# Performance work log

Measured on AMD Instinct MI355X. Metric: run time of the kernel, lower is better.

Reference implementation:

```python
import jax, jax.numpy as jnp
import numpy as np

B, T, NX, NXS, H, NY, NYS = 16384, 60, 4, 3, 64, 4, 3


def _lstm(x, h0, c0, Wih, Whh, bih, bhh):
    """PyTorch-convention LSTM (gate order i,f,g,o). x: [B,T,X]. Returns (hs [B,T,H], hT, cT)."""
    # precompute input contribution for all timesteps: [T,B,4H]
    xg = jnp.transpose(jnp.einsum('btx,gx->btg', x, Wih) + (bih + bhh), (1, 0, 2))

    def step(carry, xg_t):
        h, c = carry
        g = xg_t + h @ Whh.T
        i, f, gg, o = jnp.split(g, 4, axis=-1)
        c = jax.nn.sigmoid(f) * c + jax.nn.sigmoid(i) * jnp.tanh(gg)
        h = jax.nn.sigmoid(o) * jnp.tanh(c)
        return (h, c), h

    (hT, cT), hs = jax.lax.scan(step, (h0, c0), xg)
    return jnp.transpose(hs, (1, 0, 2)), hT, cT


def setup_inputs() -> dict:
    key = jax.random.key(0)
    ks = jax.random.split(key, 24)
    w = lambda k, shp: (jax.random.normal(k, shp, jnp.float32) * 0.1)
    return {
        'inputs_main': jax.random.normal(ks[0], (B, T, NX), jnp.float32),
        'inputs_aux': jax.random.normal(ks[1], (B, NXS), jnp.float32),
        'hx2': jax.random.normal(ks[2], (B, H), jnp.float32),
        'cx2': jax.random.normal(ks[3], (B, H), jnp.float32),
        'Ws1': w(ks[4], (H, NXS)), 'bs1': w(ks[5], (H,)),
        'Ws2': w(ks[6], (H, NXS)), 'bs2': w(ks[7], (H,)),
        'Wih1': w(ks[8], (4 * H, NX)), 'Whh1': w(ks[9], (4 * H, H)),
        'bih1': w(ks[10], (4 * H,)), 'bhh1': w(ks[11], (4 * H,)),
        'Wih2': w(ks[12], (4 * H, H)), 'Whh2': w(ks[13], (4 * H, H)),
        'bih2': w(ks[14], (4 * H,)), 'bhh2': w(ks[15], (4 * H,)),
        'Wlat': w(ks[16], (H, H)), 'blat': w(ks[17], (H,)),
        'Wout': w(ks[18], (NY, H)), 'bout': w(ks[19], (NY,)),
        'Wsfc': w(ks[20], (NYS, H)), 'bsfc': w(ks[21], (NYS,)),
    }


def reference(inputs_main, inputs_aux, hx2, cx2, Ws1, bs1, Ws2, bs2,
              Wih1, Whh1, bih1, bhh1, Wih2, Whh2, bih2, bhh2,
              Wlat, blat, Wout, bout, Wsfc, bsfc):
    # surface MLPs -> initial LSTM1 state (h raw, c tanh'd)
    hx = inputs_aux @ Ws1.T + bs1
    cx = jnp.tanh(inputs_aux @ Ws2.T + bs2)
    # run LSTM1 top-down (flipped levels)
    x1 = jnp.flip(inputs_main, axis=1)
    rnn1out, _, _ = _lstm(x1, hx, cx, Wih1, Whh1, bih1, bhh1)
    # flip back and run LSTM2 bottom-up with (hx2, cx2)
    # (the original calls rnn2 twice; only the second call's result is used)
    rnn1out_f = jnp.flip(rnn1out, axis=1)
    rnn2out, last_h, _ = _lstm(rnn1out_f, hx2, cx2, Wih2, Whh2, bih2, bhh2)
    # intermediate MLP + output head
    lat = rnn2out @ Wlat.T + blat                # [B,T,H]
    out = lat @ Wout.T + bout                    # [B,T,NY]
    out_sfc = jax.nn.relu(last_h @ Wsfc.T + bsfc)  # [B,NYS]
    return out, out_sfc
```

## Files before the change

### kernel.cpp

```cpp
#include <hip/hip_runtime.h>
#include <hip/hip_bf16.h>

#define BB 16384
#define TT 60

typedef short bf16x8 __attribute__((ext_vector_type(8)));
typedef float f32x4 __attribute__((ext_vector_type(4)));

__device__ __forceinline__ unsigned short f2bs(float f) {
    __hip_bfloat16 h = __float2bfloat16(f);
    return __builtin_bit_cast(unsigned short, h);
}

__device__ __forceinline__ unsigned cvtpk2(float lo, float hi) {
    unsigned r;
    asm("v_cvt_pk_bf16_f32 %0, %1, %2" : "=v"(r) : "v"(lo), "v"(hi));
    return r;
}

__device__ __forceinline__ void lstm_cell(float xi, float xf, float xg, float xo,
                                          float& c, float& h) {
    xi = __builtin_amdgcn_fmed3f(xi, -17.f, 17.f);
    xf = __builtin_amdgcn_fmed3f(xf, -17.f, 17.f);
    xo = __builtin_amdgcn_fmed3f(xo, -17.f, 17.f);
    xg = __builtin_amdgcn_fmed3f(xg, -11.f, 11.f);
    const float ei = __expf(-xi), ef = __expf(-xf), eo = __expf(-xo), eg = __expf(2.f * xg);
    const float di = 1.f + ei, df = 1.f + ef, dd = 1.f + eo, dg = 1.f + eg;
    const float a = di * df, b = dd * dg;
    const float R = __builtin_amdgcn_rcpf(a * b);
    const float si = df * b * R;
    const float sf = di * b * R;
    const float so = a * dg * R;
    const float tg = (eg - 1.f) * (a * dd) * R;
    const float cn = sf * c + si * tg;
    c = cn;
    const float tc = __builtin_amdgcn_fmed3f(cn, -11.f, 11.f);
    const float ec = __expf(2.f * tc);
    const float th = (ec - 1.f) * __builtin_amdgcn_rcpf(ec + 1.f);
    h = so * th;
}

#define STEP_BARRIER() do {                                   \
    asm volatile("s_waitcnt lgkmcnt(0)" ::: "memory");        \
    __builtin_amdgcn_s_barrier();                             \
    __builtin_amdgcn_sched_barrier(0);                        \
} while (0)

__device__ __forceinline__ bf16x8 pack8(float4 a, float4 b) {
    bf16x8 r;
    r[0] = (short)f2bs(a.x); r[1] = (short)f2bs(a.y);
    r[2] = (short)f2bs(a.z); r[3] = (short)f2bs(a.w);
    r[4] = (short)f2bs(b.x); r[5] = (short)f2bs(b.y);
    r[6] = (short)f2bs(b.z); r[7] = (short)f2bs(b.w);
    return r;
}

__global__ __launch_bounds__(256, 2) void k_lstm1(
    const float* __restrict__ xmain, const float* __restrict__ aux,
    const float* __restrict__ Ws1, const float* __restrict__ bs1,
    const float* __restrict__ Ws2, const float* __restrict__ bs2,
    const float* __restrict__ Wih1, const float* __restrict__ Whh1,
    const float* __restrict__ bih1, const float* __restrict__ bhh1,
    unsigned short* __restrict__ rnn1t)
{
    __shared__ unsigned short hB[2 * 4096];

    const int tid = threadIdx.x;
    {
        unsigned int* p32 = (unsigned int*)hB;
        #pragma unroll
        for (int e = 0; e < 16; ++e) p32[tid + 256 * e] = 0;
    }
    const int hj = tid >> 6, lane = tid & 63;
    const int row16 = lane & 15, quad = lane >> 4;
    const int b0 = blockIdx.x * 32;
    const int swz = (row16 & 7) << 3;

    bf16x8 wf[4][3];
    float fb[4];
    #pragma unroll
    for (int i = 0; i < 4; ++i) {
        const int g = (hj + 4 * i) * 16 + row16;
        const float* wr = Whh1 + g * 64 + quad * 8;
        wf[i][0] = pack8(*(const float4*)wr, *(const float4*)(wr + 4));
        wf[i][1] = pack8(*(const float4*)(wr + 32), *(const float4*)(wr + 36));
        float4 z4 = {0.f, 0.f, 0.f, 0.f};
        float4 xw = z4;
        if (quad == 0) xw = *(const float4*)(Wih1 + g * 4);
        wf[i][2] = pack8(xw, z4);
        fb[i] = bih1[g] + bhh1[g];
    }
    __syncthreads();

    const int j = hj * 16 + row16;
    const unsigned oA0 = (unsigned)(((row16 * 128 + 0 + quad * 8) ^ swz) * 2);
    const unsigned oA1 = (unsigned)(((row16 * 128 + 32 + quad * 8) ^ swz) * 2);
    const unsigned oA2 = (unsigned)(((row16 * 128 + 64 + quad * 8) ^ swz) * 2);
    unsigned oW[4];
    #pragma unroll
    for (int r = 0; r < 4; ++r) {
        const int m = quad * 4 + r;
        oW[r] = (unsigned)(((m * 128 + j) ^ ((m & 7) << 3)) * 2);
    }
    const unsigned oX = (unsigned)(((lane * 128 + 64) ^ ((lane & 7) << 3)) * 2);
    char* const hBb = (char*)hB;

    const float w10 = Ws1[j * 3], w11 = Ws1[j * 3 + 1], w12 = Ws1[j * 3 + 2], sb1v = bs1[j];
    const float w20 = Ws2[j * 3], w21 = Ws2[j * 3 + 1], w22 = Ws2[j * 3 + 2], sb2v = bs2[j];
    f32x4 cc[2];
    #pragma unroll
    for (int mh = 0; mh < 2; ++mh) {
        #pragma unroll
        for (int r = 0; r < 4; ++r) {
            const int m = mh * 16 + quad * 4 + r;
            const float a0v = aux[(b0 + m) * 3], a1v = aux[(b0 + m) * 3 + 1], a2v = aux[(b0 + m) * 3 + 2];
            float h0 = w10 * a0v + w11 * a1v + w12 * a2v + sb1v;
            float c0in = w20 * a0v + w21 * a1v + w22 * a2v + sb2v;
            c0in = __builtin_amdgcn_fmed3f(c0in, -11.f, 11.f);
            const float e0 = __expf(2.f * c0in);
            cc[mh][r] = (e0 - 1.f) * __builtin_amdgcn_rcpf(e0 + 1.f);
            *(unsigned short*)(hBb + oW[r] + mh * 4096) = f2bs(h0);
        }
    }
    if (hj == 2 && lane < 32) {
        float4 xv = ((const float4*)xmain)[(size_t)(b0 + lane) * TT + 59];
        uint2 p2 = { cvtpk2(xv.x, xv.y), cvtpk2(xv.z, xv.w) };
        *(uint2*)(hBb + oX) = p2;
    }
    __syncthreads();

    const float4* px = (const float4*)xmain + (size_t)(b0 + lane) * TT + 58;
    unsigned short* pst = rnn1t + ((size_t)60 * BB + b0 + ((hj >> 1) << 4) + row16) * 64 + ((hj & 1) << 5) + quad * 8;

    unsigned pofs = 0;
    #pragma unroll 1
    for (int s = 0; s < TT; ++s) {
        char* hbP = hBb + pofs;
        char* hbN = hBb + (pofs ^ 8192);
        float4 xv;
        if (hj == 2 && lane < 32 && s < TT - 1) xv = *px;
        bf16x8 a0[2], a1[2], a2[2];
        #pragma unroll
        for (int mh = 0; mh < 2; ++mh) {
            a0[mh] = *(const bf16x8*)(hbP + oA0 + mh * 4096);
            a1[mh] = *(const bf16x8*)(hbP + oA1 + mh * 4096);
            a2[mh] = *(const bf16x8*)(hbP + oA2 + mh * 4096);
        }
        if (s > 0) {
            bf16x8 sv = (hj == 0) ? a0[0] : (hj == 1) ? a1[0] : (hj == 2) ? a0[1] : a1[1];
            *(bf16x8*)pst = sv;
        }
        pst -= (size_t)BB * 64;
        px -= 1;

        f32x4 ac[2][4];
        #pragma unroll
        for (int mh = 0; mh < 2; ++mh)
            #pragma unroll
            for (int i = 0; i < 4; ++i) { f32x4 v = {fb[i], fb[i], fb[i], fb[i]}; ac[mh][i] = v; }
        #pragma unroll
        for (int mh = 0; mh < 2; ++mh) {
            #pragma unroll
            for (int i = 0; i < 4; ++i) {
                ac[mh][i] = __builtin_amdgcn_mfma_f32_16x16x32_bf16(a0[mh], wf[i][0], ac[mh][i], 0, 0, 0);
                ac[mh][i] = __builtin_amdgcn_mfma_f32_16x16x32_bf16(a1[mh], wf[i][1], ac[mh][i], 0, 0, 0);
                ac[mh][i] = __builtin_amdgcn_mfma_f32_16x16x32_bf16(a2[mh], wf[i][2], ac[mh][i], 0, 0, 0);
            }
        }
        #pragma unroll
        for (int mh = 0; mh < 2; ++mh) {
            float hr[4];
            #pragma unroll
            for (int r = 0; r < 4; ++r) {
                float cr = cc[mh][r];
                lstm_cell(ac[mh][0][r], ac[mh][1][r], ac[mh][2][r], ac[mh][3][r], cr, hr[r]);
                cc[mh][r] = cr;
            }
            const unsigned u01 = cvtpk2(hr[0], hr[1]);
            const unsigned u23 = cvtpk2(hr[2], hr[3]);
            *(unsigned short*)(hbN + oW[0] + mh * 4096) = (unsigned short)u01;
            *(unsigned short*)(hbN + oW[1] + mh * 4096) = (unsigned short)(u01 >> 16);
            *(unsigned short*)(hbN + oW[2] + mh * 4096) = (unsigned short)u23;
            *(unsigned short*)(hbN + oW[3] + mh * 4096) = (unsigned short)(u23 >> 16);
        }
        if (hj == 2 && lane < 32 && s < TT - 1) {
            uint2 p2 = { cvtpk2(xv.x, xv.y), cvtpk2(xv.z, xv.w) };
            *(uint2*)(hbN + oX) = p2;
        }
        STEP_BARRIER();
        pofs ^= 8192;
    }
    {
        char* hbP = hBb + pofs;
        bf16x8 sv;
        if (hj == 0)      sv = *(const bf16x8*)(hbP + oA0);
        else if (hj == 1) sv = *(const bf16x8*)(hbP + oA1);
        else if (hj == 2) sv = *(const bf16x8*)(hbP + oA0 + 4096);
        else              sv = *(const bf16x8*)(hbP + oA1 + 4096);
        *(bf16x8*)&rnn1t[((size_t)(b0 + ((hj >> 1) << 4) + row16)) * 64 + ((hj & 1) << 5) + quad * 8] = sv;
    }
}

__global__ __launch_bounds__(256, 2) void k_lstm2(
    const unsigned short* __restrict__ rnn1t,
    const float* __restrict__ hx2, const float* __restrict__ cx2,
    const float* __restrict__ Wih2, const float* __restrict__ Whh2,
    const float* __restrict__ bih2, const float* __restrict__ bhh2,
    const float* __restrict__ Wlat, const float* __restrict__ blat,
    const float* __restrict__ Wout, const float* __restrict__ bout,
    const float* __restrict__ Wsfc, const float* __restrict__ bsfc,
    float* __restrict__ out)
{
    __shared__ unsigned short hB[2 * 4096];
    __shared__ unsigned short whead[16 * 64];

    const int tid = threadIdx.x;
    {
        unsigned int* w32 = (unsigned int*)whead;
        w32[tid] = 0; w32[tid + 256] = 0;
    }
    const int hj = tid >> 6, lane = tid & 63;
    const int row16 = lane & 15, quad = lane >> 4;
    const int b0 = blockIdx.x * 32;
    const int swz = (row16 & 7) << 3;

    bf16x8 wf[4][4];
    float fb[4];
    #pragma unroll
    for (int i = 0; i < 4; ++i) {
        const int g = (hj + 4 * i) * 16 + row16;
        const float* wh = Whh2 + g * 64 + quad * 8;
        const float* wi = Wih2 + g * 64 + quad * 8;
        wf[i][0] = pack8(*(const float4*)wh, *(const float4*)(wh + 4));
        wf[i][1] = pack8(*(const float4*)(wh + 32), *(const float4*)(wh + 36));
        wf[i][2] = pack8(*(const float4*)wi, *(const float4*)(wi + 4));
        wf[i][3] = pack8(*(const float4*)(wi + 32), *(const float4*)(wi + 36));
        fb[i] = bih2[g] + bhh2[g];
    }
    float bcomb = 0.f;
    if (row16 < 4) {
        float s = 0.f;
        for (int jj = 0; jj < 64; ++jj) s += Wout[row16 * 64 + jj] * blat[jj];
        bcomb = s + bout[row16];
    } else if (row16 < 7) {
        bcomb = bsfc[row16 - 4];
    }
    __syncthreads();

    {
        const int o = tid >> 6, k = tid & 63;
        float s = 0.f;
        for (int jj = 0; jj < 64; ++jj) s += Wout[o * 64 + jj] * Wlat[jj * 64 + k];
        whead[(o * 64 + k) ^ ((o & 7) << 3)] = f2bs(s);
        if (tid < 192) {
            const int o2 = o + 4;
            whead[(o2 * 64 + k) ^ ((o2 & 7) << 3)] = f2bs(Wsfc[o * 64 + k]);
        }
    }

    const int j = hj * 16 + row16;
    const unsigned oA0 = (unsigned)(((row16 * 128 + 0 + quad * 8) ^ swz) * 2);
    const unsigned oA1 = (unsigned)(((row16 * 128 + 32 + quad * 8) ^ swz) * 2);
    const unsigned oA2 = (unsigned)(((row16 * 128 + 64 + quad * 8) ^ swz) * 2);
    const unsigned oA3 = (unsigned)(((row16 * 128 + 96 + quad * 8) ^ swz) * 2);
    unsigned oW[4];
    #pragma unroll
    for (int r = 0; r < 4; ++r) {
        const int m = quad * 4 + r;
        oW[r] = (unsigned)(((m * 128 + j) ^ ((m & 7) << 3)) * 2);
    }
    const unsigned oPV = (unsigned)(((row16 * 128 + 64 + ((hj & 1) << 5) + quad * 8) ^ swz) * 2);
    const unsigned oH0 = (unsigned)(((row16 * 64 + 0 + quad * 8) ^ swz) * 2);
    const unsigned oH1 = (unsigned)(((row16 * 64 + 32 + quad * 8) ^ swz) * 2);
    char* const hBb = (char*)hB;
    char* const whb = (char*)whead;

    f32x4 cc[2];
    #pragma unroll
    for (int mh = 0; mh < 2; ++mh) {
        #pragma unroll
        for (int r = 0; r < 4; ++r) {
            const int m = mh * 16 + quad * 4 + r;
            cc[mh][r] = cx2[(size_t)(b0 + m) * 64 + j];
            *(unsigned short*)(hBb + oW[r] + mh * 4096) = f2bs(hx2[(size_t)(b0 + m) * 64 + j]);
        }
    }
    if (hj < 2) {
        bf16x8 v0 = *(const bf16x8*)&rnn1t[((size_t)(b0 + row16)) * 64 + ((hj & 1) << 5) + quad * 8];
        bf16x8 v1 = *(const bf16x8*)&rnn1t[((size_t)(b0 + 16 + row16)) * 64 + ((hj & 1) << 5) + quad * 8];
        *(bf16x8*)(hBb + oPV) = v0;
        *(bf16x8*)(hBb + oPV + 4096) = v1;
    }
    __syncthreads();

    bf16x8 wh0 = *(const bf16x8*)(whb + oH0);
    bf16x8 wh1 = *(const bf16x8*)(whb + oH1);

    const unsigned short* ppv = rnn1t + ((size_t)BB + b0 + row16) * 64 + ((hj & 1) << 5) + quad * 8;
    float* po = out + ((size_t)(b0 + ((hj == 2) ? 16 : 0) + quad * 4) * TT) * 4 + row16;

    unsigned pofs = 0;
    #pragma unroll 1
    for (int t = 0; t < TT; ++t) {
        char* hbP = hBb + pofs;
        char* hbN = hBb + (pofs ^ 8192);
        bf16x8 pv0, pv1;
        if (hj < 2 && t < TT - 1) {
            pv0 = *(const bf16x8*)ppv;
            pv1 = *(const bf16x8*)(ppv + 16 * 64);
        }
        ppv += (size_t)BB * 64;

        bf16x8 a0[2], a1[2], a2[2], a3[2];
        #pragma unroll
        for (int mh = 0; mh < 2; ++mh) {
            a0[mh] = *(const bf16x8*)(hbP + oA0 + mh * 4096);
            a1[mh] = *(const bf16x8*)(hbP + oA1 + mh * 4096);
            a2[mh] = *(const bf16x8*)(hbP + oA2 + mh * 4096);
            a3[mh] = *(const bf16x8*)(hbP + oA3 + mh * 4096);
        }

        if (hj >= 2 && t > 0) {
            const bf16x8 ha0 = (hj == 3) ? a0[0] : a0[1];
            const bf16x8 ha1 = (hj == 3) ? a1[0] : a1[1];
            f32x4 hacc = {bcomb, bcomb, bcomb, bcomb};
            hacc = __builtin_amdgcn_mfma_f32_16x16x32_bf16(ha0, wh0, hacc, 0, 0, 0);
            hacc = __builtin_amdgcn_mfma_f32_16x16x32_bf16(ha1, wh1, hacc, 0, 0, 0);
            if (row16 < 4) {
                #pragma unroll
                for (int r = 0; r < 4; ++r)
                    po[r * TT * 4] = hacc[r];
            }
            po += 4;
        }

        f32x4 ac[2][4];
        #pragma unroll
        for (int mh = 0; mh < 2; ++mh)
            #pragma unroll
            for (int i = 0; i < 4; ++i) { f32x4 v = {fb[i], fb[i], fb[i], fb[i]}; ac[mh][i] = v; }
        #pragma unroll
        for (int mh = 0; mh < 2; ++mh) {
            #pragma unroll
            for (int i = 0; i < 4; ++i) {
                ac[mh][i] = __builtin_amdgcn_mfma_f32_16x16x32_bf16(a0[mh], wf[i][0], ac[mh][i], 0, 0, 0);
                ac[mh][i] = __builtin_amdgcn_mfma_f32_16x16x32_bf16(a1[mh], wf[i][1], ac[mh][i], 0, 0, 0);
                ac[mh][i] = __builtin_amdgcn_mfma_f32_16x16x32_bf16(a2[mh], wf[i][2], ac[mh][i], 0, 0, 0);
                ac[mh][i] = __builtin_amdgcn_mfma_f32_16x16x32_bf16(a3[mh], wf[i][3], ac[mh][i], 0, 0, 0);
            }
        }
        #pragma unroll
        for (int mh = 0; mh < 2; ++mh) {
            float hr[4];
            #pragma unroll
            for (int r = 0; r < 4; ++r) {
                float cr = cc[mh][r];
                lstm_cell(ac[mh][0][r], ac[mh][1][r], ac[mh][2][r], ac[mh][3][r], cr, hr[r]);
                cc[mh][r] = cr;
            }
            const unsigned u01 = cvtpk2(hr[0], hr[1]);
            const unsigned u23 = cvtpk2(hr[2], hr[3]);
            *(unsigned short*)(hbN + oW[0] + mh * 4096) = (unsigned short)u01;
            *(unsigned short*)(hbN + oW[1] + mh * 4096) = (unsigned short)(u01 >> 16);
            *(unsigned short*)(hbN + oW[2] + mh * 4096) = (unsigned short)u23;
            *(unsigned short*)(hbN + oW[3] + mh * 4096) = (unsigned short)(u23 >> 16);
        }
        if (hj < 2 && t < TT - 1) {
            *(bf16x8*)(hbN + oPV) = pv0;
            *(bf16x8*)(hbN + oPV + 4096) = pv1;
        }
        STEP_BARRIER();
        pofs ^= 8192;
    }
    if (hj >= 2) {
        char* hbP = hBb + pofs;
        const int mho = (hj == 3) ? 0 : 4096;
        bf16x8 ea0 = *(const bf16x8*)(hbP + oA0 + mho);
        bf16x8 ea1 = *(const bf16x8*)(hbP + oA1 + mho);
        f32x4 hacc = {bcomb, bcomb, bcomb, bcomb};
        hacc = __builtin_amdgcn_mfma_f32_16x16x32_bf16(ea0, wh0, hacc, 0, 0, 0);
        hacc = __builtin_amdgcn_mfma_f32_16x16x32_bf16(ea1, wh1, hacc, 0, 0, 0);
        const int rb = b0 + ((hj == 2) ? 16 : 0) + quad * 4;
        if (row16 < 4) {
            #pragma unroll
            for (int r = 0; r < 4; ++r)
                out[((size_t)(rb + r) * TT + 59) * 4 + row16] = hacc[r];
        } else if (row16 < 7) {
            float* osfc = out + (size_t)BB * TT * 4;
            #pragma unroll
            for (int r = 0; r < 4; ++r)
                osfc[(size_t)(rb + r) * 3 + (row16 - 4)] = fmaxf(hacc[r], 0.f);
        }
    }
}

extern "C" void kernel_launch(void* const* d_in, const int* in_sizes, int n_in,
                              void* d_out, int out_size, void* d_ws, size_t ws_size,
                              hipStream_t stream) {
    const float* xmain = (const float*)d_in[0];
    const float* aux   = (const float*)d_in[1];
    const float* hx2   = (const float*)d_in[2];
    const float* cx2   = (const float*)d_in[3];
    const float* Ws1   = (const float*)d_in[4];
    const float* bs1   = (const float*)d_in[5];
    const float* Ws2   = (const float*)d_in[6];
    const float* bs2   = (const float*)d_in[7];
    const float* Wih1  = (const float*)d_in[8];
    const float* Whh1  = (const float*)d_in[9];
    const float* bih1  = (const float*)d_in[10];
    const float* bhh1  = (const float*)d_in[11];
    const float* Wih2  = (const float*)d_in[12];
    const float* Whh2  = (const float*)d_in[13];
    const float* bih2  = (const float*)d_in[14];
    const float* bhh2  = (const float*)d_in[15];
    const float* Wlat  = (const float*)d_in[16];
    const float* blat  = (const float*)d_in[17];
    const float* Wout  = (const float*)d_in[18];
    const float* bout  = (const float*)d_in[19];
    const float* Wsfc  = (const float*)d_in[20];
    const float* bsfc  = (const float*)d_in[21];

    unsigned short* rnn1t = (unsigned short*)d_ws;
    float* out = (float*)d_out;

    dim3 grid(BB / 32), block(256);
    k_lstm1<<<grid, block, 0, stream>>>(xmain, aux, Ws1, bs1, Ws2, bs2,
                                        Wih1, Whh1, bih1, bhh1, rnn1t);
    k_lstm2<<<grid, block, 0, stream>>>(rnn1t, hx2, cx2, Wih2, Whh2, bih2, bhh2,
                                        Wlat, blat, Wout, bout, Wsfc, bsfc, out);
}
```

Measured before the change: 237.6 us.

## Fuse both LSTM layers into one kernel per batch tile

Merges the two LSTM kernels into a single kernel. Each 32-row batch block runs LSTM1 over all timesteps, writes the bf16 sequence to workspace, then runs LSTM2 and the output head. This removes one kernel launch and the device-wide dependency between the layers, so the two phases of different blocks can overlap across CUs. The intermediate still goes through global memory, and register pressure may rise because both phases sit in one function.

Measured after the change: 232.9 us. No clear change (-2.0%).

```diff
diff --git a/kernel.cpp b/kernel.cpp
--- a/kernel.cpp
+++ b/kernel.cpp
@@ -55,161 +55,19 @@
     return r;
 }
 
-__global__ __launch_bounds__(256, 2) void k_lstm1(
+__global__ __launch_bounds__(256, 2) void k_fused(
     const float* __restrict__ xmain, const float* __restrict__ aux,
     const float* __restrict__ Ws1, const float* __restrict__ bs1,
     const float* __restrict__ Ws2, const float* __restrict__ bs2,
     const float* __restrict__ Wih1, const float* __restrict__ Whh1,
     const float* __restrict__ bih1, const float* __restrict__ bhh1,
-    unsigned short* __restrict__ rnn1t)
-{
-    __shared__ unsigned short hB[2 * 4096];
-
-    const int tid = threadIdx.x;
-    {
-        unsigned int* p32 = (unsigned int*)hB;
-        #pragma unroll
-        for (int e = 0; e < 16; ++e) p32[tid + 256 * e] = 0;
-    }
-    const int hj = tid >> 6, lane = tid & 63;
-    const int row16 = lane & 15, quad = lane >> 4;
-    const int b0 = blockIdx.x * 32;
-    const int swz = (row16 & 7) << 3;
-
-    bf16x8 wf[4][3];
-    float fb[4];
-    #pragma unroll
-    for (int i = 0; i < 4; ++i) {
-        const int g = (hj + 4 * i) * 16 + row16;
-        const float* wr = Whh1 + g * 64 + quad * 8;
-        wf[i][0] = pack8(*(const float4*)wr, *(const float4*)(wr + 4));
-        wf[i][1] = pack8(*(const float4*)(wr + 32), *(const float4*)(wr + 36));
-        float4 z4 = {0.f, 0.f, 0.f, 0.f};
-        float4 xw = z4;
-        if (quad == 0) xw = *(const float4*)(Wih1 + g * 4);
-        wf[i][2] = pack8(xw, z4);
-        fb[i] = bih1[g] + bhh1[g];
-    }
-    __syncthreads();
-
-    const int j = hj * 16 + row16;
-    const unsigned oA0 = (unsigned)(((row16 * 128 + 0 + quad * 8) ^ swz) * 2);
-    const unsigned oA1 = (unsigned)(((row16 * 128 + 32 + quad * 8) ^ swz) * 2);
-    const unsigned oA2 = (unsigned)(((row16 * 128 + 64 + quad * 8) ^ swz) * 2);
-    unsigned oW[4];
-    #pragma unroll
-    for (int r = 0; r < 4; ++r) {
-        const int m = quad * 4 + r;
-        oW[r] = (unsigned)(((m * 128 + j) ^ ((m & 7) << 3)) * 2);
-    }
-    const unsigned oX = (unsigned)(((lane * 128 + 64) ^ ((lane & 7) << 3)) * 2);
-    char* const hBb = (char*)hB;
-
-    const float w10 = Ws1[j * 3], w11 = Ws1[j * 3 + 1], w12 = Ws1[j * 3 + 2], sb1v = bs1[j];
-    const float w20 = Ws2[j * 3], w21 = Ws2[j * 3 + 1], w22 = Ws2[j * 3 + 2], sb2v = bs2[j];
-    f32x4 cc[2];
-    #pragma unroll
-    for (int mh = 0; mh < 2; ++mh) {
-        #pragma unroll
-        for (int r = 0; r < 4; ++r) {
-            const int m = mh * 16 + quad * 4 + r;
-            const float a0v = aux[(b0 + m) * 3], a1v = aux[(b0 + m) * 3 + 1], a2v = aux[(b0 + m) * 3 + 2];
-            float h0 = w10 * a0v + w11 * a1v + w12 * a2v + sb1v;
-            float c0in = w20 * a0v + w21 * a1v + w22 * a2v + sb2v;
-            c0in = __builtin_amdgcn_fmed3f(c0in, -11.f, 11.f);
-            const float e0 = __expf(2.f * c0in);
-            cc[mh][r] = (e0 - 1.f) * __builtin_amdgcn_rcpf(e0 + 1.f);
-            *(unsigned short*)(hBb + oW[r] + mh * 4096) = f2bs(h0);
-        }
-    }
-    if (hj == 2 && lane < 32) {
-        float4 xv = ((const float4*)xmain)[(size_t)(b0 + lane) * TT + 59];
-        uint2 p2 = { cvtpk2(xv.x, xv.y), cvtpk2(xv.z, xv.w) };
-        *(uint2*)(hBb + oX) = p2;
-    }
-    __syncthreads();
-
-    const float4* px = (const float4*)xmain + (size_t)(b0 + lane) * TT + 58;
-    unsigned short* pst = rnn1t + ((size_t)60 * BB + b0 + ((hj >> 1) << 4) + row16) * 64 + ((hj & 1) << 5) + quad * 8;
-
-    unsigned pofs = 0;
-    #pragma unroll 1
-    for (int s = 0; s < TT; ++s) {
-        char* hbP = hBb + pofs;
-        char* hbN = hBb + (pofs ^ 8192);
-        float4 xv;
-        if (hj == 2 && lane < 32 && s < TT - 1) xv = *px;
-        bf16x8 a0[2], a1[2], a2[2];
-        #pragma unroll
-        for (int mh = 0; mh < 2; ++mh) {
-            a0[mh] = *(const bf16x8*)(hbP + oA0 + mh * 4096);
-            a1[mh] = *(const bf16x8*)(hbP + oA1 + mh * 4096);
-            a2[mh] = *(const bf16x8*)(hbP + oA2 + mh * 4096);
-        }
-        if (s > 0) {
-            bf16x8 sv = (hj == 0) ? a0[0] : (hj == 1) ? a1[0] : (hj == 2) ? a0[1] : a1[1];
-            *(bf16x8*)pst = sv;
-        }
-        pst -= (size_t)BB * 64;
-        px -= 1;
-
-        f32x4 ac[2][4];
-        #pragma unroll
-        for (int mh = 0; mh < 2; ++mh)
-            #pragma unroll
-            for (int i = 0; i < 4; ++i) { f32x4 v = {fb[i], fb[i], fb[i], fb[i]}; ac[mh][i] = v; }
-        #pragma unroll
-        for (int mh = 0; mh < 2; ++mh) {
-            #pragma unroll
-            for (int i = 0; i < 4; ++i) {
-                ac[mh][i] = __builtin_amdgcn_mfma_f32_16x16x32_bf16(a0[mh], wf[i][0], ac[mh][i], 0, 0, 0);
-                ac[mh][i] = __builtin_amdgcn_mfma_f32_16x16x32_bf16(a1[mh], wf[i][1], ac[mh][i], 0, 0, 0);
-                ac[mh][i] = __builtin_amdgcn_mfma_f32_16x16x32_bf16(a2[mh], wf[i][2], ac[mh][i], 0, 0, 0);
-            }
-        }
-        #pragma unroll
-        for (int mh = 0; mh < 2; ++mh) {
-            float hr[4];
-            #pragma unroll
-            for (int r = 0; r < 4; ++r) {
-                float cr = cc[mh][r];
-                lstm_cell(ac[mh][0][r], ac[mh][1][r], ac[mh][2][r], ac[mh][3][r], cr, hr[r]);
-                cc[mh][r] = cr;
-            }
-            const unsigned u01 = cvtpk2(hr[0], hr[1]);
-            const unsigned u23 = cvtpk2(hr[2], hr[3]);
-            *(unsigned short*)(hbN + oW[0] + mh * 4096) = (unsigned short)u01;
-            *(unsigned short*)(hbN + oW[1] + mh * 4096) = (unsigned short)(u01 >> 16);
-            *(unsigned short*)(hbN + oW[2] + mh * 4096) = (unsigned short)u23;
-            *(unsigned short*)(hbN + oW[3] + mh * 4096) = (unsigned short)(u23 >> 16);
-        }
-        if (hj == 2 && lane < 32 && s < TT - 1) {
-            uint2 p2 = { cvtpk2(xv.x, xv.y), cvtpk2(xv.z, xv.w) };
-            *(uint2*)(hbN + oX) = p2;
-        }
-        STEP_BARRIER();
-        pofs ^= 8192;
-    }
-    {
-        char* hbP = hBb + pofs;
-        bf16x8 sv;
-        if (hj == 0)      sv = *(const bf16x8*)(hbP + oA0);
-        else if (hj == 1) sv = *(const bf16x8*)(hbP + oA1);
-        else if (hj == 2) sv = *(const bf16x8*)(hbP + oA0 + 4096);
-        else              sv = *(const bf16x8*)(hbP + oA1 + 4096);
-        *(bf16x8*)&rnn1t[((size_t)(b0 + ((hj >> 1) << 4) + row16)) * 64 + ((hj & 1) << 5) + quad * 8] = sv;
-    }
-}
-
-__global__ __launch_bounds__(256, 2) void k_lstm2(
-    const unsigned short* __restrict__ rnn1t,
     const float* __restrict__ hx2, const float* __restrict__ cx2,
     const float* __restrict__ Wih2, const float* __restrict__ Whh2,
     const float* __restrict__ bih2, const float* __restrict__ bhh2,
     const float* __restrict__ Wlat, const float* __restrict__ blat,
     const float* __restrict__ Wout, const float* __restrict__ bout,
     const float* __restrict__ Wsfc, const float* __restrict__ bsfc,
-    float* __restrict__ out)
+    unsigned short* __restrict__ rnn1t, float* __restrict__ out)
 {
     __shared__ unsigned short hB[2 * 4096];
     __shared__ unsigned short whead[16 * 64];
@@ -223,40 +81,8 @@
     const int row16 = lane & 15, quad = lane >> 4;
     const int b0 = blockIdx.x * 32;
     const int swz = (row16 & 7) << 3;
-
-    bf16x8 wf[4][4];
-    float fb[4];
-    #pragma unroll
-    for (int i = 0; i < 4; ++i) {
-        const int g = (hj + 4 * i) * 16 + row16;
-        const float* wh = Whh2 + g * 64 + quad * 8;
-        const float* wi = Wih2 + g * 64 + quad * 8;
-        wf[i][0] = pack8(*(const float4*)wh, *(const float4*)(wh + 4));
-        wf[i][1] = pack8(*(const float4*)(wh + 32), *(const float4*)(wh + 36));
-        wf[i][2] = pack8(*(const float4*)wi, *(const float4*)(wi + 4));
-        wf[i][3] = pack8(*(const float4*)(wi + 32), *(const float4*)(wi + 36));
-        fb[i] = bih2[g] + bhh2[g];
-    }
-    float bcomb = 0.f;
-    if (row16 < 4) {
-        float s = 0.f;
-        for (int jj = 0; jj < 64; ++jj) s += Wout[row16 * 64 + jj] * blat[jj];
-        bcomb = s + bout[row16];
-    } else if (row16 < 7) {
-        bcomb = bsfc[row16 - 4];
-    }
-    __syncthreads();
-
-    {
-        const int o = tid >> 6, k = tid & 63;
-        float s = 0.f;
-        for (int jj = 0; jj < 64; ++jj) s += Wout[o * 64 + jj] * Wlat[jj * 64 + k];
-        whead[(o * 64 + k) ^ ((o & 7) << 3)] = f2bs(s);
-        if (tid < 192) {
-            const int o2 = o + 4;
-            whead[(o2 * 64 + k) ^ ((o2 & 7) << 3)] = f2bs(Wsfc[o * 64 + k]);
-        }
-    }
+    char* const hBb = (char*)hB;
+    char* const whb = (char*)whead;
 
     const int j = hj * 16 + row16;
     const unsigned oA0 = (unsigned)(((row16 * 128 + 0 + quad * 8) ^ swz) * 2);
@@ -269,127 +95,282 @@
         const int m = quad * 4 + r;
         oW[r] = (unsigned)(((m * 128 + j) ^ ((m & 7) << 3)) * 2);
     }
-    const unsigned oPV = (unsigned)(((row16 * 128 + 64 + ((hj & 1) << 5) + quad * 8) ^ swz) * 2);
-    const unsigned oH0 = (unsigned)(((row16 * 64 + 0 + quad * 8) ^ swz) * 2);
-    const unsigned oH1 = (unsigned)(((row16 * 64 + 32 + quad * 8) ^ swz) * 2);
-    char* const hBb = (char*)hB;
-    char* const whb = (char*)whead;
-
-    f32x4 cc[2];
-    #pragma unroll
-    for (int mh = 0; mh < 2; ++mh) {
+
+    {
+        {
+            unsigned int* p32 = (unsigned int*)hB;
+            #pragma unroll
+            for (int e = 0; e < 16; ++e) p32[tid + 256 * e] = 0;
+        }
+        bf16x8 wf[4][3];
+        float fb[4];
         #pragma unroll
-        for (int r = 0; r < 4; ++r) {
-            const int m = mh * 16 + quad * 4 + r;
-            cc[mh][r] = cx2[(size_t)(b0 + m) * 64 + j];
-            *(unsigned short*)(hBb + oW[r] + mh * 4096) = f2bs(hx2[(size_t)(b0 + m) * 64 + j]);
-        }
-    }
-    if (hj < 2) {
-        bf16x8 v0 = *(const bf16x8*)&rnn1t[((size_t)(b0 + row16)) * 64 + ((hj & 1) << 5) + quad * 8];
-        bf16x8 v1 = *(const bf16x8*)&rnn1t[((size_t)(b0 + 16 + row16)) * 64 + ((hj & 1) << 5) + quad * 8];
-        *(bf16x8*)(hBb + oPV) = v0;
-        *(bf16x8*)(hBb + oPV + 4096) = v1;
-    }
-    __syncthreads();
-
-    bf16x8 wh0 = *(const bf16x8*)(whb + oH0);
-    bf16x8 wh1 = *(const bf16x8*)(whb + oH1);
-
-    const unsigned short* ppv = rnn1t + ((size_t)BB + b0 + row16) * 64 + ((hj & 1) << 5) + quad * 8;
-    float* po = out + ((size_t)(b0 + ((hj == 2) ? 16 : 0) + quad * 4) * TT) * 4 + row16;
-
-    unsigned pofs = 0;
-    #pragma unroll 1
-    for (int t = 0; t < TT; ++t) {
-        char* hbP = hBb + pofs;
-        char* hbN = hBb + (pofs ^ 8192);
-        bf16x8 pv0, pv1;
-        if (hj < 2 && t < TT - 1) {
-            pv0 = *(const bf16x8*)ppv;
-            pv1 = *(const bf16x8*)(ppv + 16 * 64);
-        }
-        ppv += (size_t)BB * 64;
-
-        bf16x8 a0[2], a1[2], a2[2], a3[2];
+        for (int i = 0; i < 4; ++i) {
+            const int g = (hj + 4 * i) * 16 + row16;
+            const float* wr = Whh1 + g * 64 + quad * 8;
+            wf[i][0] = pack8(*(const float4*)wr, *(const float4*)(wr + 4));
+            wf[i][1] = pack8(*(const float4*)(wr + 32), *(const float4*)(wr + 36));
+            float4 z4 = {0.f, 0.f, 0.f, 0.f};
+            float4 xw = z4;
+            if (quad == 0) xw = *(const float4*)(Wih1 + g * 4);
+            wf[i][2] = pack8(xw, z4);
+            fb[i] = bih1[g] + bhh1[g];
+        }
+        __syncthreads();
+
+        const unsigned oX = (unsigned)(((lane * 128 + 64) ^ ((lane & 7) << 3)) * 2);
+
+        const float w10 = Ws1[j * 3], w11 = Ws1[j * 3 + 1], w12 = Ws1[j * 3 + 2], sb1v = bs1[j];
+        const float w20 = Ws2[j * 3], w21 = Ws2[j * 3 + 1], w22 = Ws2[j * 3 + 2], sb2v = bs2[j];
+        f32x4 cc[2];
         #pragma unroll
         for (int mh = 0; mh < 2; ++mh) {
-            a0[mh] = *(const bf16x8*)(hbP + oA0 + mh * 4096);
-            a1[mh] = *(const bf16x8*)(hbP + oA1 + mh * 4096);
-            a2[mh] = *(const bf16x8*)(hbP + oA2 + mh * 4096);
-            a3[mh] = *(const bf16x8*)(hbP + oA3 + mh * 4096);
-        }
-
-        if (hj >= 2 && t > 0) {
-            const bf16x8 ha0 = (hj == 3) ? a0[0] : a0[1];
-            const bf16x8 ha1 = (hj == 3) ? a1[0] : a1[1];
-            f32x4 hacc = {bcomb, bcomb, bcomb, bcomb};
-            hacc = __builtin_amdgcn_mfma_f32_16x16x32_bf16(ha0, wh0, hacc, 0, 0, 0);
-            hacc = __builtin_amdgcn_mfma_f32_16x16x32_bf16(ha1, wh1, hacc, 0, 0, 0);
-            if (row16 < 4) {
-                #pragma unroll
-                for (int r = 0; r < 4; ++r)
-                    po[r * TT * 4] = hacc[r];
-            }
-            po += 4;
-        }
-
-        f32x4 ac[2][4];
+            #pragma unroll
+            for (int r = 0; r < 4; ++r) {
+                const int m = mh * 16 + quad * 4 + r;
+                const float a0v = aux[(b0 + m) * 3], a1v = aux[(b0 + m) * 3 + 1], a2v = aux[(b0 + m) * 3 + 2];
+                float h0 = w10 * a0v + w11 * a1v + w12 * a2v + sb1v;
+                float c0in = w20 * a0v + w21 * a1v + w22 * a2v + sb2v;
+                c0in = __builtin_amdgcn_fmed3f(c0in, -11.f, 11.f);
+                const float e0 = __expf(2.f * c0in);
+                cc[mh][r] = (e0 - 1.f) * __builtin_amdgcn_rcpf(e0 + 1.f);
+                *(unsigned short*)(hBb + oW[r] + mh * 4096) = f2bs(h0);
+            }
+        }
+        if (hj == 2 && lane < 32) {
+            float4 xv = ((const float4*)xmain)[(size_t)(b0 + lane) * TT + 59];
+            uint2 p2 = { cvtpk2(xv.x, xv.y), cvtpk2(xv.z, xv.w) };
+            *(uint2*)(hBb + oX) = p2;
+        }
+        __syncthreads();
+
+        const float4* px = (const float4*)xmain + (size_t)(b0 + lane) * TT + 58;
+        unsigned short* pst = rnn1t + ((size_t)60 * BB + b0 + ((hj >> 1) << 4) + row16) * 64 + ((hj & 1) << 5) + quad * 8;
+
+        unsigned pofs = 0;
+        #pragma unroll 1
+        for (int s = 0; s < TT; ++s) {
+            char* hbP = hBb + pofs;
+            char* hbN = hBb + (pofs ^ 8192);
+            float4 xv;
+            if (hj == 2 && lane < 32 && s < TT - 1) xv = *px;
+            bf16x8 a0[2], a1[2], a2[2];
+            #pragma unroll
+            for (int mh = 0; mh < 2; ++mh) {
+                a0[mh] = *(const bf16x8*)(hbP + oA0 + mh * 4096);
+                a1[mh] = *(const bf16x8*)(hbP + oA1 + mh * 4096);
+                a2[mh] = *(const bf16x8*)(hbP + oA2 + mh * 4096);
+            }
+            if (s > 0) {
+                bf16x8 sv = (hj == 0) ? a0[0] : (hj == 1) ? a1[0] : (hj == 2) ? a0[1] : a1[1];
+                *(bf16x8*)pst = sv;
+            }
+            pst -= (size_t)BB * 64;
+            px -= 1;
+
+            f32x4 ac[2][4];
+            #pragma unroll
+            for (int mh = 0; mh < 2; ++mh)
+                #pragma unroll
+                for (int i = 0; i < 4; ++i) { f32x4 v = {fb[i], fb[i], fb[i], fb[i]}; ac[mh][i] = v; }
+            #pragma unroll
+            for (int mh = 0; mh < 2; ++mh) {
+                #pragma unroll
+                for (int i = 0; i < 4; ++i) {
+                    ac[mh][i] = __builtin_amdgcn_mfma_f32_16x16x32_bf16(a0[mh], wf[i][0], ac[mh][i], 0, 0, 0);
+                    ac[mh][i] = __builtin_amdgcn_mfma_f32_16x16x32_bf16(a1[mh], wf[i][1], ac[mh][i], 0, 0, 0);
+                    ac[mh][i] = __builtin_amdgcn_mfma_f32_16x16x32_bf16(a2[mh], wf[i][2], ac[mh][i], 0, 0, 0);
+                }
+            }
+            #pragma unroll
+            for (int mh = 0; mh < 2; ++mh) {
+                float hr[4];
+                #pragma unroll
+                for (int r = 0; r < 4; ++r) {
+                    float cr = cc[mh][r];
+                    lstm_cell(ac[mh][0][r], ac[mh][1][r], ac[mh][2][r], ac[mh][3][r], cr, hr[r]);
+                    cc[mh][r] = cr;
+                }
+                const unsigned u01 = cvtpk2(hr[0], hr[1]);
+                const unsigned u23 = cvtpk2(hr[2], hr[3]);
+                *(unsigned short*)(hbN + oW[0] + mh * 4096) = (unsigned short)u01;
+                *(unsigned short*)(hbN + oW[1] + mh * 4096) = (unsigned short)(u01 >> 16);
+                *(unsigned short*)(hbN + oW[2] + mh * 4096) = (unsigned short)u23;
+                *(unsigned short*)(hbN + oW[3] + mh * 4096) = (unsigned short)(u23 >> 16);
+            }
+            if (hj == 2 && lane < 32 && s < TT - 1) {
+                uint2 p2 = { cvtpk2(xv.x, xv.y), cvtpk2(xv.z, xv.w) };
+                *(uint2*)(hbN + oX) = p2;
+            }
+            STEP_BARRIER();
+            pofs ^= 8192;
+        }
+        {
+            char* hbP = hBb + pofs;
+            bf16x8 sv;
+            if (hj == 0)      sv = *(const bf16x8*)(hbP + oA0);
+            else if (hj == 1) sv = *(const bf16x8*)(hbP + oA1);
+            else if (hj == 2) sv = *(const bf16x8*)(hbP + oA0 + 4096);
+            else              sv = *(const bf16x8*)(hbP + oA1 + 4096);
+            *(bf16x8*)&rnn1t[((size_t)(b0 + ((hj >> 1) << 4) + row16)) * 64 + ((hj & 1) << 5) + quad * 8] = sv;
+        }
+    }
+
+    __syncthreads();
+
+    {
+        bf16x8 wf[4][4];
+        float fb[4];
         #pragma unroll
-        for (int mh = 0; mh < 2; ++mh)
-            #pragma unroll
-            for (int i = 0; i < 4; ++i) { f32x4 v = {fb[i], fb[i], fb[i], fb[i]}; ac[mh][i] = v; }
+        for (int i = 0; i < 4; ++i) {
+            const int g = (hj + 4 * i) * 16 + row16;
+            const float* wh = Whh2 + g * 64 + quad * 8;
+            const float* wi = Wih2 + g * 64 + quad * 8;
+            wf[i][0] = pack8(*(const float4*)wh, *(const float4*)(wh + 4));
+            wf[i][1] = pack8(*(const float4*)(wh + 32), *(const float4*)(wh + 36));
+            wf[i][2] = pack8(*(const float4*)wi, *(const float4*)(wi + 4));
+            wf[i][3] = pack8(*(const float4*)(wi + 32), *(const float4*)(wi + 36));
+            fb[i] = bih2[g] + bhh2[g];
+        }
+        float bcomb = 0.f;
+        if (row16 < 4) {
+            float ss = 0.f;
+            for (int jj = 0; jj < 64; ++jj) ss += Wout[row16 * 64 + jj] * blat[jj];
+            bcomb = ss + bout[row16];
+        } else if (row16 < 7) {
+            bcomb = bsfc[row16 - 4];
+        }
+        {
+            const int o = tid >> 6, k = tid & 63;
+            float ss = 0.f;
+            for (int jj = 0; jj < 64; ++jj) ss += Wout[o * 64 + jj] * Wlat[jj * 64 + k];
+            whead[(o * 64 + k) ^ ((o & 7) << 3)] = f2bs(ss);
+            if (tid < 192) {
+                const int o2 = o + 4;
+                whead[(o2 * 64 + k) ^ ((o2 & 7) << 3)] = f2bs(Wsfc[o * 64 + k]);
+            }
+        }
+
+        const unsigned oPV = (unsigned)(((row16 * 128 + 64 + ((hj & 1) << 5) + quad * 8) ^ swz) * 2);
+        const unsigned oH0 = (unsigned)(((row16 * 64 + 0 + quad * 8) ^ swz) * 2);
+        const unsigned oH1 = (unsigned)(((row16 * 64 + 32 + quad * 8) ^ swz) * 2);
+
+        f32x4 cc[2];
         #pragma unroll
         for (int mh = 0; mh < 2; ++mh) {
             #pragma unroll
-            for (int i = 0; i < 4; ++i) {
-                ac[mh][i] = __builtin_amdgcn_mfma_f32_16x16x32_bf16(a0[mh], wf[i][0], ac[mh][i], 0, 0, 0);
-                ac[mh][i] = __builtin_amdgcn_mfma_f32_16x16x32_bf16(a1[mh], wf[i][1], ac[mh][i], 0, 0, 0);
-                ac[mh][i] = __builtin_amdgcn_mfma_f32_16x16x32_bf16(a2[mh], wf[i][2], ac[mh][i], 0, 0, 0);
-                ac[mh][i] = __builtin_amdgcn_mfma_f32_16x16x32_bf16(a3[mh], wf[i][3], ac[mh][i], 0, 0, 0);
-            }
-        }
-        #pragma unroll
-        for (int mh = 0; mh < 2; ++mh) {
-            float hr[4];
-            #pragma unroll
             for (int r = 0; r < 4; ++r) {
-                float cr = cc[mh][r];
-                lstm_cell(ac[mh][0][r], ac[mh][1][r], ac[mh][2][r], ac[mh][3][r], cr, hr[r]);
-                cc[mh][r] = cr;
-            }
-            const unsigned u01 = cvtpk2(hr[0], hr[1]);
-            const unsigned u23 = cvtpk2(hr[2], hr[3]);
-            *(unsigned short*)(hbN + oW[0] + mh * 4096) = (unsigned short)u01;
-            *(unsigned short*)(hbN + oW[1] + mh * 4096) = (unsigned short)(u01 >> 16);
-            *(unsigned short*)(hbN + oW[2] + mh * 4096) = (unsigned short)u23;
-            *(unsigned short*)(hbN + oW[3] + mh * 4096) = (unsigned short)(u23 >> 16);
-        }
-        if (hj < 2 && t < TT - 1) {
-            *(bf16x8*)(hbN + oPV) = pv0;
-            *(bf16x8*)(hbN + oPV + 4096) = pv1;
-        }
-        STEP_BARRIER();
-        pofs ^= 8192;
-    }
-    if (hj >= 2) {
-        char* hbP = hBb + pofs;
-        const int mho = (hj == 3) ? 0 : 4096;
-        bf16x8 ea0 = *(const bf16x8*)(hbP + oA0 + mho);
-        bf16x8 ea1 = *(const bf16x8*)(hbP + oA1 + mho);
-        f32x4 hacc = {bcomb, bcomb, bcomb, bcomb};
-        hacc = __builtin_amdgcn_mfma_f32_16x16x32_bf16(ea0, wh0, hacc, 0, 0, 0);
-        hacc = __builtin_amdgcn_mfma_f32_16x16x32_bf16(ea1, wh1, hacc, 0, 0, 0);
-        const int rb = b0 + ((hj == 2) ? 16 : 0) + quad * 4;
-        if (row16 < 4) {
-            #pragma unroll
-            for (int r = 0; r < 4; ++r)
-                out[((size_t)(rb + r) * TT + 59) * 4 + row16] = hacc[r];
-        } else if (row16 < 7) {
-            float* osfc = out + (size_t)BB * TT * 4;
-            #pragma unroll
-            for (int r = 0; r < 4; ++r)
-                osfc[(size_t)(rb + r) * 3 + (row16 - 4)] = fmaxf(hacc[r], 0.f);
+                const int m = mh * 16 + quad * 4 + r;
+                cc[mh][r] = cx2[(size_t)(b0 + m) * 64 + j];
+                *(unsigned short*)(hBb + oW[r] + mh * 4096) = f2bs(hx2[(size_t)(b0 + m) * 64 + j]);
+            }
+        }
+        if (hj < 2) {
+            bf16x8 v0 = *(const bf16x8*)&rnn1t[((size_t)(b0 + row16)) * 64 + ((hj & 1) << 5) + quad * 8];
+            bf16x8 v1 = *(const bf16x8*)&rnn1t[((size_t)(b0 + 16 + row16)) * 64 + ((hj & 1) << 5) + quad * 8];
+            *(bf16x8*)(hBb + oPV) = v0;
+            *(bf16x8*)(hBb + oPV + 4096) = v1;
+        }
+        __syncthreads();
+
+        bf16x8 wh0 = *(const bf16x8*)(whb + oH0);
+        bf16x8 wh1 = *(const bf16x8*)(whb + oH1);
+
+        const unsigned short* ppv = rnn1t + ((size_t)BB + b0 + row16) * 64 + ((hj & 1) << 5) + quad * 8;
+        float* po = out + ((size_t)(b0 + ((hj == 2) ? 16 : 0) + quad * 4) * TT) * 4 + row16;
+
+        unsigned pofs = 0;
+        #pragma unroll 1
+        for (int t = 0; t < TT; ++t) {
+            char* hbP = hBb + pofs;
+            char* hbN = hBb + (pofs ^ 8192);
+            bf16x8 pv0, pv1;
+            if (hj < 2 && t < TT - 1) {
+                pv0 = *(const bf16x8*)ppv;
+                pv1 = *(const bf16x8*)(ppv + 16 * 64);
+            }
+            ppv += (size_t)BB * 64;
+
+            bf16x8 a0[2], a1[2], a2[2], a3[2];
+            #pragma unroll
+            for (int mh = 0; mh < 2; ++mh) {
+                a0[mh] = *(const bf16x8*)(hbP + oA0 + mh * 4096);
+                a1[mh] = *(const bf16x8*)(hbP + oA1 + mh * 4096);
+                a2[mh] = *(const bf16x8*)(hbP + oA2 + mh * 4096);
+                a3[mh] = *(const bf16x8*)(hbP + oA3 + mh * 4096);
+            }
+
+            if (hj >= 2 && t > 0) {
+                const bf16x8 ha0 = (hj == 3) ? a0[0] : a0[1];
+                const bf16x8 ha1 = (hj == 3) ? a1[0] : a1[1];
+                f32x4 hacc = {bcomb, bcomb, bcomb, bcomb};
+                hacc = __builtin_amdgcn_mfma_f32_16x16x32_bf16(ha0, wh0, hacc, 0, 0, 0);
+                hacc = __builtin_amdgcn_mfma_f32_16x16x32_bf16(ha1, wh1, hacc, 0, 0, 0);
+                if (row16 < 4) {
+                    #pragma unroll
+                    for (int r = 0; r < 4; ++r)
+                        po[r * TT * 4] = hacc[r];
+                }
+                po += 4;
+            }
+
+            f32x4 ac[2][4];
+            #pragma unroll
+            for (int mh = 0; mh < 2; ++mh)
+                #pragma unroll
+                for (int i = 0; i < 4; ++i) { f32x4 v = {fb[i], fb[i], fb[i], fb[i]}; ac[mh][i] = v; }
+            #pragma unroll
+            for (int mh = 0; mh < 2; ++mh) {
+                #pragma unroll
+                for (int i = 0; i < 4; ++i) {
+                    ac[mh][i] = __builtin_amdgcn_mfma_f32_16x16x32_bf16(a0[mh], wf[i][0], ac[mh][i], 0, 0, 0);
+                    ac[mh][i] = __builtin_amdgcn_mfma_f32_16x16x32_bf16(a1[mh], wf[i][1], ac[mh][i], 0, 0, 0);
+                    ac[mh][i] = __builtin_amdgcn_mfma_f32_16x16x32_bf16(a2[mh], wf[i][2], ac[mh][i], 0, 0, 0);
+                    ac[mh][i] = __builtin_amdgcn_mfma_f32_16x16x32_bf16(a3[mh], wf[i][3], ac[mh][i], 0, 0, 0);
+                }
+            }
+            #pragma unroll
+            for (int mh = 0; mh < 2; ++mh) {
+                float hr[4];
+                #pragma unroll
+                for (int r = 0; r < 4; ++r) {
+                    float cr = cc[mh][r];
+                    lstm_cell(ac[mh][0][r], ac[mh][1][r], ac[mh][2][r], ac[mh][3][r], cr, hr[r]);
+                    cc[mh][r] = cr;
+                }
+                const unsigned u01 = cvtpk2(hr[0], hr[1]);
+                const unsigned u23 = cvtpk2(hr[2], hr[3]);
+                *(unsigned short*)(hbN + oW[0] + mh * 4096) = (unsigned short)u01;
+                *(unsigned short*)(hbN + oW[1] + mh * 4096) = (unsigned short)(u01 >> 16);
+                *(unsigned short*)(hbN + oW[2] + mh * 4096) = (unsigned short)u23;
+                *(unsigned short*)(hbN + oW[3] + mh * 4096) = (unsigned short)(u23 >> 16);
+            }
+            if (hj < 2 && t < TT - 1) {
+                *(bf16x8*)(hbN + oPV) = pv0;
+                *(bf16x8*)(hbN + oPV + 4096) = pv1;
+            }
+            STEP_BARRIER();
+            pofs ^= 8192;
+        }
+        if (hj >= 2) {
+            char* hbP = hBb + pofs;
+            const int mho = (hj == 3) ? 0 : 4096;
+            bf16x8 ea0 = *(const bf16x8*)(hbP + oA0 + mho);
+            bf16x8 ea1 = *(const bf16x8*)(hbP + oA1 + mho);
+            f32x4 hacc = {bcomb, bcomb, bcomb, bcomb};
+            hacc = __builtin_amdgcn_mfma_f32_16x16x32_bf16(ea0, wh0, hacc, 0, 0, 0);
+            hacc = __builtin_amdgcn_mfma_f32_16x16x32_bf16(ea1, wh1, hacc, 0, 0, 0);
+            const int rb = b0 + ((hj == 2) ? 16 : 0) + quad * 4;
+            if (row16 < 4) {
+                #pragma unroll
+                for (int r = 0; r < 4; ++r)
+                    out[((size_t)(rb + r) * TT + 59) * 4 + row16] = hacc[r];
+            } else if (row16 < 7) {
+                float* osfc = out + (size_t)BB * TT * 4;
+                #pragma unroll
+                for (int r = 0; r < 4; ++r)
+                    osfc[(size_t)(rb + r) * 3 + (row16 - 4)] = fmaxf(hacc[r], 0.f);
+            }
         }
     }
 }
@@ -424,8 +405,9 @@
     float* out = (float*)d_out;
 
     dim3 grid(BB / 32), block(256);
-    k_lstm1<<<grid, block, 0, stream>>>(xmain, aux, Ws1, bs1, Ws2, bs2,
-                                        Wih1, Whh1, bih1, bhh1, rnn1t);
-    k_lstm2<<<grid, block, 0, stream>>>(rnn1t, hx2, cx2, Wih2, Whh2, bih2, bhh2,
-                                        Wlat, blat, Wout, bout, Wsfc, bsfc, out);
-}
+    k_fused<<<grid, block, 0, stream>>>(xmain, aux, Ws1, bs1, Ws2, bs2,
+                                        Wih1, Whh1, bih1, bhh1,
+                                        hx2, cx2, Wih2, Whh2, bih2, bhh2,
+                                        Wlat, blat, Wout, bout, Wsfc, bsfc,
+                                        rnn1t, out);
+}
```
